# Optimization experiments

Measured on AMD Instinct MI355X. Metric: run time of the kernel, lower is better.

The kernel has to match this reference:

```python
import jax, jax.numpy as jnp
import numpy as np

N_ENT = 50000
N_REL = 16
N_EDGE = 1000000
D = 64


def setup_inputs() -> dict:
    key = jax.random.key(0)
    ks = jax.random.split(key, 20)
    inp = {
        'ent_embed': jax.random.normal(ks[0], (N_ENT, D), jnp.float32) * 0.1,
        'rel_embed': jax.random.normal(ks[1], (N_REL, D), jnp.float32) * 0.1,
        'W_R': jax.random.normal(ks[2], (N_REL, D, D), jnp.float32) * 0.1,
        'W1_0': jax.random.normal(ks[3], (64, 64), jnp.float32) * 0.1,
        'b1_0': jax.random.normal(ks[4], (64,), jnp.float32) * 0.1,
        'W2_0': jax.random.normal(ks[5], (64, 64), jnp.float32) * 0.1,
        'b2_0': jax.random.normal(ks[6], (64,), jnp.float32) * 0.1,
        'W1_1': jax.random.normal(ks[7], (64, 32), jnp.float32) * 0.1,
        'b1_1': jax.random.normal(ks[8], (32,), jnp.float32) * 0.1,
        'W2_1': jax.random.normal(ks[9], (64, 32), jnp.float32) * 0.1,
        'b2_1': jax.random.normal(ks[10], (32,), jnp.float32) * 0.1,
        'W1_2': jax.random.normal(ks[11], (32, 16), jnp.float32) * 0.1,
        'b1_2': jax.random.normal(ks[12], (16,), jnp.float32) * 0.1,
        'W2_2': jax.random.normal(ks[13], (32, 16), jnp.float32) * 0.1,
        'b2_2': jax.random.normal(ks[14], (16,), jnp.float32) * 0.1,
        'src': jax.random.randint(ks[15], (N_EDGE,), 0, N_ENT, jnp.int32),
        'dst': jax.random.randint(ks[16], (N_EDGE,), 0, N_ENT, jnp.int32),
        'etype': jax.random.randint(ks[17], (N_EDGE,), 0, N_REL, jnp.int32),
    }
    return inp


def _l2_normalize(x, eps=1e-12):
    # matches torch F.normalize(p=2, dim=1)
    n = jnp.sqrt(jnp.sum(x * x, axis=1, keepdims=True))
    return x / jnp.maximum(n, eps)


def _kgat_forward(ent_embed, rel_embed, W_R, layer_params, src, dst, etype):
    N = ent_embed.shape[0]
    # --- compute_attention: per-relation TransR projection of all entities ---
    # equivalent to per-edge ent[src] @ W_R[type] without materializing [E, D, D]
    proj = jnp.einsum('nd,rde->rne', ent_embed, W_R)          # [R, N, D]
    r_mul_t = proj[etype, src]                                # [E, D] (tail = src)
    r_mul_h = proj[etype, dst]                                # [E, D] (head = dst)
    att = jnp.sum(r_mul_t * jnp.tanh(r_mul_h + rel_embed[etype]), axis=-1)  # [E]
    # edge softmax grouped by destination node
    m = jax.ops.segment_max(att, dst, num_segments=N)         # [N]
    e = jnp.exp(att - m[dst])
    s = jax.ops.segment_sum(e, dst, num_segments=N)           # [N]
    a = e / s[dst]                                            # [E]

    # --- cf_embedding: bi-interaction aggregator layers ---
    h = ent_embed
    all_embed = [h]
    for (W1, b1, W2, b2) in layer_params:
        msg = a[:, None] * h[src]                             # [E, d_in]
        N_h = jax.ops.segment_sum(msg, dst, num_segments=N)   # [N, d_in]
        out = (jax.nn.leaky_relu((h + N_h) @ W1 + b1, 0.01)
               + jax.nn.leaky_relu((h * N_h) @ W2 + b2, 0.01))
        h = out
        all_embed.append(_l2_normalize(out))
    return jnp.concatenate(all_embed, axis=1)                 # [N, 64+64+32+16=176]


def reference(ent_embed, rel_embed, W_R,
              W1_0, b1_0, W2_0, b2_0,
              W1_1, b1_1, W2_1, b2_1,
              W1_2, b1_2, W2_2, b2_2,
              src, dst, etype):
    layer_params = [(W1_0, b1_0, W2_0, b2_0),
                    (W1_1, b1_1, W2_1, b2_1),
                    (W1_2, b1_2, W2_2, b2_2)]
    return _kgat_forward(ent_embed, rel_embed, W_R, layer_params, src, dst, etype)
```

## Files before the change

kernel.cpp:

```cpp
#include <hip/hip_runtime.h>
#include <hip/hip_bf16.h>
#include <cmath>

#define N_ENT  50000
#define N_RELS 16
#define N_EDGE 1000000
#define DIM    64
#define OUT_STRIDE 176

typedef float f32x4 __attribute__((ext_vector_type(4)));
typedef short s16x8 __attribute__((ext_vector_type(8)));
typedef uint  u32x4 __attribute__((ext_vector_type(4)));

__device__ inline void bf16x8_unpack(uint4 u, float* f) {
    f[0] = __uint_as_float((u.x & 0xffffu) << 16);
    f[1] = __uint_as_float(u.x & 0xffff0000u);
    f[2] = __uint_as_float((u.y & 0xffffu) << 16);
    f[3] = __uint_as_float(u.y & 0xffff0000u);
    f[4] = __uint_as_float((u.z & 0xffffu) << 16);
    f[5] = __uint_as_float(u.z & 0xffff0000u);
    f[6] = __uint_as_float((u.w & 0xffffu) << 16);
    f[7] = __uint_as_float(u.w & 0xffff0000u);
}

__device__ inline ushort f2bf(float x) {
    __hip_bfloat16 b = __float2bfloat16(x);
    return *(ushort*)&b;
}

__device__ inline uint cvt_pk_bf16(float lo, float hi) {
    uint r;
    asm("v_cvt_pk_bf16_f32 %0, %1, %2" : "=v"(r) : "v"(lo), "v"(hi));
    return r;
}

__device__ __host__ inline int pcol(int p) {
    int qp = (p >> 3) & 7;
    int k  = p & 7;
    return 16 * (k >> 1) + 2 * qp + (k & 1);
}

__global__ __launch_bounds__(256) void prep_convert_kernel(
        const float* __restrict__ ent,
        ushort* __restrict__ ent_pi,
        float* __restrict__ out) {
    int i = blockIdx.x * blockDim.x + threadIdx.x;
    if (i < N_ENT * DIM) {
        float v = ent[i];
        ushort b = f2bf(v);
        int n = i >> 6, c = i & 63;
        int pos = ((c & 15) >> 1) * 8 + ((c >> 4) << 1) + (c & 1);
        ent_pi[(size_t)n * 64 + pos] = b;
        out[(size_t)n * OUT_STRIDE + c] = v;
    }
}

__global__ __launch_bounds__(256) void scan1_kernel(
        const int* __restrict__ counts, int* __restrict__ excl,
        int* __restrict__ bsum, int n) {
    __shared__ int sh[256];
    int t = threadIdx.x;
    int i = blockIdx.x * 256 + t;
    int c = (i < n) ? counts[i] : 0;
    sh[t] = c;
    __syncthreads();
    for (int off = 1; off < 256; off <<= 1) {
        int v = (t >= off) ? sh[t - off] : 0;
        __syncthreads();
        sh[t] += v;
        __syncthreads();
    }
    if (i < n) excl[i] = sh[t] - c;
    if (t == 255) bsum[blockIdx.x] = sh[255];
}

__global__ __launch_bounds__(256) void scan2_kernel(
        const int* __restrict__ bsum, int* __restrict__ boff,
        int* __restrict__ row_ptr, int nb, int n) {
    __shared__ int sh[256];
    int t = threadIdx.x;
    int v = (t < nb) ? bsum[t] : 0;
    sh[t] = v;
    __syncthreads();
    for (int off = 1; off < 256; off <<= 1) {
        int x = (t >= off) ? sh[t - off] : 0;
        __syncthreads();
        sh[t] += x;
        __syncthreads();
    }
    if (t < nb) boff[t] = sh[t] - v;
    if (t == nb - 1) row_ptr[n] = sh[t];
}

__global__ __launch_bounds__(256) void scan3_pos_kernel(
        const int* __restrict__ excl, const int* __restrict__ boff,
        int* __restrict__ row_ptr,
        const int* __restrict__ src, const int* __restrict__ dst,
        const int* __restrict__ etype, const int* __restrict__ off,
        unsigned long long* __restrict__ einfo) {
    int i = blockIdx.x * blockDim.x + threadIdx.x;
    if (i < N_ENT) row_ptr[i] = excl[i] + boff[i >> 8];
    if (i < N_EDGE) {
        int d = dst[i];
        int pos = excl[d] + boff[d >> 8] + off[i];
        unsigned long long info =
              (unsigned long long)(unsigned)src[i]
            | ((unsigned long long)(unsigned)d << 16)
            | ((unsigned long long)(unsigned)etype[i] << 32);
        einfo[pos] = info;
    }
}

__device__ __forceinline__ void gz_body(
        int r, int wid, int nw, int lane,
        const ushort* __restrict__ ent_pi,
        const float*  __restrict__ W_R,
        const float*  __restrict__ rel,
        ushort* __restrict__ Z,
        float* __restrict__ myLds) {
    int m = lane & 15;
    int q = lane >> 4;

    const float* Wr = W_R + (size_t)r * DIM * DIM;
    s16x8 b1[4][2], b2[4][2];
#pragma unroll
    for (int c = 0; c < 4; ++c)
#pragma unroll
        for (int ch = 0; ch < 2; ++ch)
#pragma unroll
            for (int j = 0; j < 8; ++j) {
                b1[c][ch][j] = (short)f2bf(Wr[pcol(ch * 32 + q * 8 + j) * DIM + c * 16 + m]);
                b2[c][ch][j] = (short)f2bf(Wr[(c * 16 + m) * DIM + ch * 32 + q * 8 + j]);
            }
    float relv[4];
#pragma unroll
    for (int c = 0; c < 4; ++c) relv[c] = rel[r * DIM + c * 16 + m];

    int par = m & 1;
    const int ntiles = N_ENT / 16;

    for (int t = wid; t < ntiles; t += nw) {
        int row0 = t * 16;
        const s16x8* arow = (const s16x8*)(ent_pi + (size_t)(row0 + m) * DIM);
        s16x8 a0 = arow[q];
        s16x8 a1 = arow[4 + q];
        f32x4 acc[4];
#pragma unroll
        for (int c = 0; c < 4; ++c) acc[c] = (f32x4){0.f, 0.f, 0.f, 0.f};
#pragma unroll
        for (int c = 0; c < 4; ++c) {
            acc[c] = __builtin_amdgcn_mfma_f32_16x16x32_bf16(a0, b1[c][0], acc[c], 0, 0, 0);
            acc[c] = __builtin_amdgcn_mfma_f32_16x16x32_bf16(a1, b1[c][1], acc[c], 0, 0, 0);
        }
#pragma unroll
        for (int c = 0; c < 4; ++c)
#pragma unroll
            for (int i = 0; i < 4; ++i) {
                float x = acc[c][i] + relv[c];
                float e2 = __expf(2.f * x);
                float g = 1.f - 2.f * __builtin_amdgcn_rcpf(e2 + 1.f);
                myLds[(q * 4 + i) * 68 + c * 16 + m] = g;
            }
        union { uint u[4]; s16x8 v; } a2u[2];
#pragma unroll
        for (int ch = 0; ch < 2; ++ch) {
            const f32x4* gp = (const f32x4*)(myLds + m * 68 + ch * 32 + q * 8);
            f32x4 g0 = gp[0];
            f32x4 g1 = gp[1];
            a2u[ch].u[0] = cvt_pk_bf16(g0[0], g0[1]);
            a2u[ch].u[1] = cvt_pk_bf16(g0[2], g0[3]);
            a2u[ch].u[2] = cvt_pk_bf16(g1[0], g1[1]);
            a2u[ch].u[3] = cvt_pk_bf16(g1[2], g1[3]);
        }

        f32x4 zacc[4];
#pragma unroll
        for (int c = 0; c < 4; ++c) zacc[c] = (f32x4){0.f, 0.f, 0.f, 0.f};
#pragma unroll
        for (int c = 0; c < 4; ++c) {
            zacc[c] = __builtin_amdgcn_mfma_f32_16x16x32_bf16(a2u[0].v, b2[c][0], zacc[c], 0, 0, 0);
            zacc[c] = __builtin_amdgcn_mfma_f32_16x16x32_bf16(a2u[1].v, b2[c][1], zacc[c], 0, 0, 0);
        }

        int rowA = row0 + 4 * q + (par ? 2 : 0);
        ushort* zb = Z + ((size_t)r * N_ENT + rowA) * 64 + (m >> 1) * 8;
#pragma unroll
        for (int rep = 0; rep < 2; ++rep) {
            u32x4 Wv;
#pragma unroll
            for (int c = 0; c < 4; ++c) {
                float send = par ? zacc[c][rep] : zacc[c][2 + rep];
                float own  = par ? zacc[c][2 + rep] : zacc[c][rep];
                float oth  = __shfl_xor(send, 1, 64);
                float lo = par ? oth : own;
                float hi = par ? own : oth;
                Wv[c] = cvt_pk_bf16(lo, hi);
            }
            __builtin_nontemporal_store(Wv, (u32x4*)(zb + rep * 64));
        }
    }
}

#define HIST_LANES 131072

__global__ __launch_bounds__(256, 4) void gz_hist_kernel(
        const ushort* __restrict__ ent_pi,
        const float*  __restrict__ W_R,
        const float*  __restrict__ rel,
        ushort* __restrict__ Z,
        const int* __restrict__ dst,
        int* __restrict__ counts,
        int* __restrict__ off) {
    __shared__ __align__(16) float lds[3][16 * 68 + 16];
    int lane = threadIdx.x & 63;
    int wv   = threadIdx.x >> 6;

    if (wv == 3) {
        int lane_gid = blockIdx.x * 64 + lane;
        int d[8]; bool v[8]; int o[8];
#pragma unroll
        for (int k = 0; k < 8; ++k) {
            int i = lane_gid + k * HIST_LANES;
            v[k] = (i < N_EDGE);
            d[k] = v[k] ? dst[i] : 0;
        }
#pragma unroll
        for (int k = 0; k < 8; ++k)
            if (v[k]) o[k] = atomicAdd(&counts[d[k]], 1);
#pragma unroll
        for (int k = 0; k < 8; ++k)
            if (v[k]) off[lane_gid + k * HIST_LANES] = o[k];
        return;
    }

    int r   = blockIdx.x >> 7;
    int xb  = blockIdx.x & 127;
    int wid = xb * 3 + wv;
    gz_body(r, wid, 384, lane, ent_pi, W_R, rel, Z, lds[wv]);
}

__global__ __launch_bounds__(256) void att_dot_kernel(
        const ushort* __restrict__ ent_pi,
        const ushort* __restrict__ Z,
        const unsigned long long* __restrict__ einfo,
        uint2* __restrict__ es_csr,
        int n_edge) {
    int tid  = blockIdx.x * blockDim.x + threadIdx.x;
    int lane = threadIdx.x & 63;
    int sub  = lane >> 3;
    int q    = lane & 7;
    int base = (tid >> 6) * 64;
    if (base >= n_edge) return;

    int e[8];
    unsigned long long inf[8];
#pragma unroll
    for (int k = 0; k < 8; ++k) {
        e[k] = base + k * 8 + sub;
        inf[k] = (e[k] < n_edge) ? einfo[e[k]] : 0ull;
    }

    uint4 uz[8], ue[8];
#pragma unroll
    for (int k = 0; k < 8; ++k) {
        int s = (int)(inf[k] & 0xffffu);
        int d = (int)((inf[k] >> 16) & 0xffffu);
        int r = (int)((inf[k] >> 32) & 0xfu);
        uz[k] = *(const uint4*)(Z + ((size_t)r * N_ENT + d) * DIM + q * 8);
        ue[k] = *(const uint4*)(ent_pi + (size_t)s * DIM + q * 8);
    }

    float pr[8];
#pragma unroll
    for (int k = 0; k < 8; ++k) {
        float zv[8], ev[8];
        bf16x8_unpack(uz[k], zv);
        bf16x8_unpack(ue[k], ev);
        float p = 0.f;
#pragma unroll
        for (int j = 0; j < 8; ++j) p = fmaf(ev[j], zv[j], p);
        pr[k] = p;
    }
#pragma unroll
    for (int k = 0; k < 8; ++k) {
        pr[k] += __shfl_xor(pr[k], 1, 64);
        pr[k] += __shfl_xor(pr[k], 2, 64);
        pr[k] += __shfl_xor(pr[k], 4, 64);
    }

    if (q == 0) {
#pragma unroll
        for (int k = 0; k < 8; ++k)
            if (e[k] < n_edge)
                es_csr[e[k]] = make_uint2(__float_as_uint(pr[k]),
                                          (unsigned)(inf[k] & 0xffffu));
    }
}

__global__ __launch_bounds__(256) void agg64s_kernel(
        const ushort* __restrict__ tab,
        const uint2* __restrict__ es_csr,
        const int* __restrict__ row_ptr,
        float2* __restrict__ stats,
        float* __restrict__ N_h, int n_node) {
    int wid  = (blockIdx.x * blockDim.x + threadIdx.x) >> 6;
    int lane = threadIdx.x & 63;
    if (wid >= n_node) return;
    int q   = lane & 7;
    int sub = lane >> 3;

    int start = row_ptr[wid], end = row_ptr[wid + 1];

    float mx = -INFINITY;
    for (int i = start + lane; i < end; i += 64)
        mx = fmaxf(mx, __uint_as_float(es_csr[i].x));
#pragma unroll
    for (int o = 32; o > 0; o >>= 1)
        mx = fmaxf(mx, __shfl_xor(mx, o, 64));
    float ssum = 0.f;
    for (int i = start + lane; i < end; i += 64)
        ssum += __expf(__uint_as_float(es_csr[i].x) - mx);
#pragma unroll
    for (int o = 32; o > 0; o >>= 1)
        ssum += __shfl_xor(ssum, o, 64);
    float inv = (end > start) ? (1.0f / ssum) : 0.f;
    if (lane == 0) stats[wid] = make_float2(mx, inv);

    float acc[8];
#pragma unroll
    for (int j = 0; j < 8; ++j) acc[j] = 0.f;

    for (int p = start + sub; p < end; p += 8) {
        uint2 es = es_csr[p];
        float av = __expf(__uint_as_float(es.x) - mx);
        int   si = (int)es.y;
        uint4 u  = *(const uint4*)(tab + (size_t)si * 64 + q * 8);
        float g[8];
        bf16x8_unpack(u, g);
#pragma unroll
        for (int j = 0; j < 8; ++j) acc[j] = fmaf(av, g[j], acc[j]);
    }
#pragma unroll
    for (int mask = 8; mask < 64; mask <<= 1)
#pragma unroll
        for (int j = 0; j < 8; ++j)
            acc[j] += __shfl_xor(acc[j], mask, 64);

    if (sub == 0) {
        float* dstp = N_h + (size_t)wid * 64 + q * 8;
        *(float4*)(dstp)     = (float4){acc[0] * inv, acc[1] * inv, acc[2] * inv, acc[3] * inv};
        *(float4*)(dstp + 4) = (float4){acc[4] * inv, acc[5] * inv, acc[6] * inv, acc[7] * inv};
    }
}

__global__ __launch_bounds__(256) void agg64_kernel(
        const ushort* __restrict__ tab,
        const uint2* __restrict__ es_csr,
        const int* __restrict__ row_ptr,
        const float2* __restrict__ stats,
        float* __restrict__ N_h, int n_node) {
    int wid  = (blockIdx.x * blockDim.x + threadIdx.x) >> 6;
    int lane = threadIdx.x & 63;
    if (wid >= n_node) return;
    int q   = lane & 7;
    int sub = lane >> 3;

    int start = row_ptr[wid], end = row_ptr[wid + 1];
    float2 st = stats[wid];
    float mx = st.x, inv = st.y;
    float acc[8];
#pragma unroll
    for (int j = 0; j < 8; ++j) acc[j] = 0.f;

    for (int p = start + sub; p < end; p += 8) {
        uint2 es = es_csr[p];
        float av = __expf(__uint_as_float(es.x) - mx);
        int   si = (int)es.y;
        uint4 u  = *(const uint4*)(tab + (size_t)si * 64 + q * 8);
        float g[8];
        bf16x8_unpack(u, g);
#pragma unroll
        for (int j = 0; j < 8; ++j) acc[j] = fmaf(av, g[j], acc[j]);
    }
#pragma unroll
    for (int mask = 8; mask < 64; mask <<= 1)
#pragma unroll
        for (int j = 0; j < 8; ++j)
            acc[j] += __shfl_xor(acc[j], mask, 64);

    if (sub == 0) {
        float* dstp = N_h + (size_t)wid * 64 + q * 8;
        *(float4*)(dstp)     = (float4){acc[0] * inv, acc[1] * inv, acc[2] * inv, acc[3] * inv};
        *(float4*)(dstp + 4) = (float4){acc[4] * inv, acc[5] * inv, acc[6] * inv, acc[7] * inv};
    }
}

__global__ __launch_bounds__(256) void agg32_kernel(
        const ushort* __restrict__ tab,
        const uint2* __restrict__ es_csr,
        const int* __restrict__ row_ptr,
        const float2* __restrict__ stats,
        float* __restrict__ N_h, int n_node) {
    int wid  = (blockIdx.x * blockDim.x + threadIdx.x) >> 6;
    int lane = threadIdx.x & 63;
    if (wid >= n_node) return;
    int q   = lane & 3;
    int sub = lane >> 2;

    int start = row_ptr[wid], end = row_ptr[wid + 1];
    float2 st = stats[wid];
    float mx = st.x, inv = st.y;
    float acc[8];
#pragma unroll
    for (int j = 0; j < 8; ++j) acc[j] = 0.f;

    for (int p = start + sub; p < end; p += 16) {
        uint2 es = es_csr[p];
        float av = __expf(__uint_as_float(es.x) - mx);
        int   si = (int)es.y;
        uint4 u  = *(const uint4*)(tab + (size_t)si * 32 + q * 8);
        float g[8];
        bf16x8_unpack(u, g);
#pragma unroll
        for (int j = 0; j < 8; ++j) acc[j] = fmaf(av, g[j], acc[j]);
    }
#pragma unroll
    for (int mask = 4; mask < 64; mask <<= 1)
#pragma unroll
        for (int j = 0; j < 8; ++j)
            acc[j] += __shfl_xor(acc[j], mask, 64);

    if (sub == 0) {
        float* dstp = N_h + (size_t)wid * 32 + q * 8;
        *(float4*)(dstp)     = (float4){acc[0] * inv, acc[1] * inv, acc[2] * inv, acc[3] * inv};
        *(float4*)(dstp + 4) = (float4){acc[4] * inv, acc[5] * inv, acc[6] * inv, acc[7] * inv};
    }
}

template <int D_IN, int D_OUT, bool PERM>
__global__ __launch_bounds__(256) void mlp_mfma_kernel(
        const ushort* __restrict__ h,
        const float* __restrict__ N_h,
        const float* __restrict__ W1, const float* __restrict__ b1,
        const float* __restrict__ W2, const float* __restrict__ b2,
        ushort* __restrict__ ho,
        float* __restrict__ out_buf, int out_col) {
    constexpr int CH = D_IN / 32;
    constexpr int CT = D_OUT / 16;

    int lane = threadIdx.x & 63;
    int m    = lane & 15;
    int q    = lane >> 4;
    int wid  = blockIdx.x * (blockDim.x >> 6) + (threadIdx.x >> 6);
    int nw   = gridDim.x * (blockDim.x >> 6);

    s16x8 bu[CT][CH], bv[CT][CH];
#pragma unroll
    for (int c = 0; c < CT; ++c)
#pragma unroll
        for (int ch = 0; ch < CH; ++ch)
#pragma unroll
            for (int j = 0; j < 8; ++j) {
                int p = ch * 32 + q * 8 + j;
                int k = PERM ? pcol(p) : p;
                bu[c][ch][j] = (short)f2bf(W1[k * D_OUT + c * 16 + m]);
                bv[c][ch][j] = (short)f2bf(W2[k * D_OUT + c * 16 + m]);
            }

    const int ntiles = N_ENT / 16;
    for (int t = wid; t < ntiles; t += nw) {
        int row0 = t * 16;
        s16x8 au[CH], av[CH];
#pragma unroll
        for (int ch = 0; ch < CH; ++ch) {
            uint4 hu = *(const uint4*)(h + (size_t)(row0 + m) * D_IN + ch * 32 + q * 8);
            float hv8[8];
            bf16x8_unpack(hu, hv8);
            const float4* np = (const float4*)(N_h + (size_t)(row0 + m) * D_IN + ch * 32 + q * 8);
            float4 na = np[0], nb = np[1];
            float nv[8] = {na.x, na.y, na.z, na.w, nb.x, nb.y, nb.z, nb.w};
#pragma unroll
            for (int j = 0; j < 8; ++j) {
                au[ch][j] = (short)f2bf(hv8[j] + nv[j]);
                av[ch][j] = (short)f2bf(hv8[j] * nv[j]);
            }
        }

        f32x4 accu[CT], accv[CT];
#pragma unroll
        for (int c = 0; c < CT; ++c) {
            accu[c] = (f32x4){0.f, 0.f, 0.f, 0.f};
            accv[c] = (f32x4){0.f, 0.f, 0.f, 0.f};
        }
#pragma unroll
        for (int c = 0; c < CT; ++c)
#pragma unroll
            for (int ch = 0; ch < CH; ++ch) {
                accu[c] = __builtin_amdgcn_mfma_f32_16x16x32_bf16(au[ch], bu[c][ch], accu[c], 0, 0, 0);
                accv[c] = __builtin_amdgcn_mfma_f32_16x16x32_bf16(av[ch], bv[c][ch], accv[c], 0, 0, 0);
            }

        float res[CT][4];
        float sq[4] = {0.f, 0.f, 0.f, 0.f};
#pragma unroll
        for (int c = 0; c < CT; ++c) {
            float bb1 = b1[c * 16 + m];
            float bb2 = b2[c * 16 + m];
#pragma unroll
            for (int i = 0; i < 4; ++i) {
                float o1 = accu[c][i] + bb1;
                float o2 = accv[c][i] + bb2;
                float r1 = (o1 >= 0.f) ? o1 : 0.01f * o1;
                float r2 = (o2 >= 0.f) ? o2 : 0.01f * o2;
                float rr = r1 + r2;
                res[c][i] = rr;
                sq[i] = fmaf(rr, rr, sq[i]);
            }
        }
#pragma unroll
        for (int mask = 1; mask < 16; mask <<= 1)
#pragma unroll
            for (int i = 0; i < 4; ++i)
                sq[i] += __shfl_xor(sq[i], mask, 64);

#pragma unroll
        for (int i = 0; i < 4; ++i) {
            int row = row0 + q * 4 + i;
            float inv = 1.f / fmaxf(sqrtf(sq[i]), 1e-12f);
#pragma unroll
            for (int c = 0; c < CT; ++c) {
                int col = c * 16 + m;
                out_buf[(size_t)row * OUT_STRIDE + out_col + col] = res[c][i] * inv;
                if (ho) ho[(size_t)row * D_OUT + col] = f2bf(res[c][i]);
            }
        }
    }
}

extern "C" void kernel_launch(void* const* d_in, const int* in_sizes, int n_in,
                              void* d_out, int out_size, void* d_ws, size_t ws_size,
                              hipStream_t stream) {
    const float* ent  = (const float*)d_in[0];
    const float* rel  = (const float*)d_in[1];
    const float* W_R  = (const float*)d_in[2];
    const float* W1_0 = (const float*)d_in[3];
    const float* b1_0 = (const float*)d_in[4];
    const float* W2_0 = (const float*)d_in[5];
    const float* b2_0 = (const float*)d_in[6];
    const float* W1_1 = (const float*)d_in[7];
    const float* b1_1 = (const float*)d_in[8];
    const float* W2_1 = (const float*)d_in[9];
    const float* b2_1 = (const float*)d_in[10];
    const float* W1_2 = (const float*)d_in[11];
    const float* b1_2 = (const float*)d_in[12];
    const float* W2_2 = (const float*)d_in[13];
    const float* b2_2 = (const float*)d_in[14];
    const int*   src   = (const int*)d_in[15];
    const int*   dst   = (const int*)d_in[16];
    const int*   etype = (const int*)d_in[17];
    float* out = (float*)d_out;

    char* w = (char*)d_ws;
    uint2*  es_csr  = (uint2*)w;  w += (size_t)N_EDGE * 8;
    int*    counts  = (int*)w;    w += (size_t)(N_ENT + 64) * 4;
    int*    row_ptr = (int*)w;    w += (size_t)(N_ENT + 64) * 4;
    float2* stats   = (float2*)w; w += (size_t)(N_ENT + 64) * 8;
    int*    excl    = (int*)w;    w += (size_t)(N_ENT + 64) * 4;
    int*    bsum    = (int*)w;    w += 256 * 4;
    int*    boff    = (int*)w;    w += 256 * 4;
    ushort* ent_pi  = (ushort*)w; w += (size_t)N_ENT * 64 * 2;
    ushort* h1      = (ushort*)w; w += (size_t)N_ENT * 64 * 2;
    ushort* h2      = (ushort*)w; w += (size_t)N_ENT * 32 * 2;
    float*  N_h     = (float*)w;  w += (size_t)N_ENT * 64 * 4;
    ushort* Z       = (ushort*)w;
    (void)ws_size;

    int* off = (int*)es_csr;
    unsigned long long* einfo = (unsigned long long*)N_h;

    hipMemsetAsync(counts, 0, (size_t)N_ENT * 4, stream);

    const int nb = (N_ENT + 255) / 256;

    prep_convert_kernel<<<(N_ENT * DIM + 255) / 256, 256, 0, stream>>>(
        ent, ent_pi, out);

    gz_hist_kernel<<<2048, 256, 0, stream>>>(
        ent_pi, W_R, rel, Z, dst, counts, off);

    scan1_kernel<<<nb, 256, 0, stream>>>(counts, excl, bsum, N_ENT);
    scan2_kernel<<<1, 256, 0, stream>>>(bsum, boff, row_ptr, nb, N_ENT);
    scan3_pos_kernel<<<(N_EDGE + 255) / 256, 256, 0, stream>>>(
        excl, boff, row_ptr, src, dst, etype, off, einfo);

    att_dot_kernel<<<((N_EDGE + 63) / 64 * 64 + 255) / 256, 256, 0, stream>>>(
        ent_pi, Z, einfo, es_csr, N_EDGE);

    const int aggGrid = (N_ENT + 3) / 4;
    const int mlpGrid = 782;

    agg64s_kernel<<<aggGrid, 256, 0, stream>>>(ent_pi, es_csr, row_ptr, stats, N_h, N_ENT);
    mlp_mfma_kernel<64, 64, true><<<mlpGrid, 256, 0, stream>>>(
        ent_pi, N_h, W1_0, b1_0, W2_0, b2_0, h1, out, 64);

    agg64_kernel<<<aggGrid, 256, 0, stream>>>(h1, es_csr, row_ptr, stats, N_h, N_ENT);
    mlp_mfma_kernel<64, 32, false><<<mlpGrid, 256, 0, stream>>>(
        h1, N_h, W1_1, b1_1, W2_1, b2_1, h2, out, 128);

    agg32_kernel<<<aggGrid, 256, 0, stream>>>(h2, es_csr, row_ptr, stats, N_h, N_ENT);
    mlp_mfma_kernel<32, 16, false><<<mlpGrid, 256, 0, stream>>>(
        h2, N_h, W1_2, b1_2, W2_2, b2_2, nullptr, out, 160);
}
```

Baseline: 358.5 us.

## Fuse neighbor aggregation with bi-interaction MLP per node

Merges each layer's aggregation kernel and MFMA MLP kernel into one persistent kernel. Each wavefront aggregates one node's neighbours, stages h and N_h in shared memory, and computes the small MLP with scalar FMAs against bf16 weights held in LDS. This removes the fp32 N_h round trip through global memory and three kernel launches. In exchange it drops MFMA for scalar dot products and adds weight staging into LDS in every block. The LDS handoff relies only on an lgkmcnt wait, with no barrier, for intra-wave visibility. einfo gets its own workspace buffer now that N_h is gone.

```diff
diff --git a/kernel.cpp b/kernel.cpp
--- a/kernel.cpp
+++ b/kernel.cpp
@@ -297,242 +297,132 @@
     }
 }
 
-__global__ __launch_bounds__(256) void agg64s_kernel(
+template <int D_IN, int D_OUT, bool STATS, bool PERM>
+__global__ __launch_bounds__(256) void agg_mlp_kernel(
         const ushort* __restrict__ tab,
         const uint2* __restrict__ es_csr,
         const int* __restrict__ row_ptr,
         float2* __restrict__ stats,
-        float* __restrict__ N_h, int n_node) {
-    int wid  = (blockIdx.x * blockDim.x + threadIdx.x) >> 6;
-    int lane = threadIdx.x & 63;
-    if (wid >= n_node) return;
-    int q   = lane & 7;
-    int sub = lane >> 3;
-
-    int start = row_ptr[wid], end = row_ptr[wid + 1];
-
-    float mx = -INFINITY;
-    for (int i = start + lane; i < end; i += 64)
-        mx = fmaxf(mx, __uint_as_float(es_csr[i].x));
-#pragma unroll
-    for (int o = 32; o > 0; o >>= 1)
-        mx = fmaxf(mx, __shfl_xor(mx, o, 64));
-    float ssum = 0.f;
-    for (int i = start + lane; i < end; i += 64)
-        ssum += __expf(__uint_as_float(es_csr[i].x) - mx);
-#pragma unroll
-    for (int o = 32; o > 0; o >>= 1)
-        ssum += __shfl_xor(ssum, o, 64);
-    float inv = (end > start) ? (1.0f / ssum) : 0.f;
-    if (lane == 0) stats[wid] = make_float2(mx, inv);
-
-    float acc[8];
-#pragma unroll
-    for (int j = 0; j < 8; ++j) acc[j] = 0.f;
-
-    for (int p = start + sub; p < end; p += 8) {
-        uint2 es = es_csr[p];
-        float av = __expf(__uint_as_float(es.x) - mx);
-        int   si = (int)es.y;
-        uint4 u  = *(const uint4*)(tab + (size_t)si * 64 + q * 8);
-        float g[8];
-        bf16x8_unpack(u, g);
-#pragma unroll
-        for (int j = 0; j < 8; ++j) acc[j] = fmaf(av, g[j], acc[j]);
-    }
-#pragma unroll
-    for (int mask = 8; mask < 64; mask <<= 1)
-#pragma unroll
-        for (int j = 0; j < 8; ++j)
-            acc[j] += __shfl_xor(acc[j], mask, 64);
-
-    if (sub == 0) {
-        float* dstp = N_h + (size_t)wid * 64 + q * 8;
-        *(float4*)(dstp)     = (float4){acc[0] * inv, acc[1] * inv, acc[2] * inv, acc[3] * inv};
-        *(float4*)(dstp + 4) = (float4){acc[4] * inv, acc[5] * inv, acc[6] * inv, acc[7] * inv};
-    }
-}
-
-__global__ __launch_bounds__(256) void agg64_kernel(
-        const ushort* __restrict__ tab,
-        const uint2* __restrict__ es_csr,
-        const int* __restrict__ row_ptr,
-        const float2* __restrict__ stats,
-        float* __restrict__ N_h, int n_node) {
-    int wid  = (blockIdx.x * blockDim.x + threadIdx.x) >> 6;
-    int lane = threadIdx.x & 63;
-    if (wid >= n_node) return;
-    int q   = lane & 7;
-    int sub = lane >> 3;
-
-    int start = row_ptr[wid], end = row_ptr[wid + 1];
-    float2 st = stats[wid];
-    float mx = st.x, inv = st.y;
-    float acc[8];
-#pragma unroll
-    for (int j = 0; j < 8; ++j) acc[j] = 0.f;
-
-    for (int p = start + sub; p < end; p += 8) {
-        uint2 es = es_csr[p];
-        float av = __expf(__uint_as_float(es.x) - mx);
-        int   si = (int)es.y;
-        uint4 u  = *(const uint4*)(tab + (size_t)si * 64 + q * 8);
-        float g[8];
-        bf16x8_unpack(u, g);
-#pragma unroll
-        for (int j = 0; j < 8; ++j) acc[j] = fmaf(av, g[j], acc[j]);
-    }
-#pragma unroll
-    for (int mask = 8; mask < 64; mask <<= 1)
-#pragma unroll
-        for (int j = 0; j < 8; ++j)
-            acc[j] += __shfl_xor(acc[j], mask, 64);
-
-    if (sub == 0) {
-        float* dstp = N_h + (size_t)wid * 64 + q * 8;
-        *(float4*)(dstp)     = (float4){acc[0] * inv, acc[1] * inv, acc[2] * inv, acc[3] * inv};
-        *(float4*)(dstp + 4) = (float4){acc[4] * inv, acc[5] * inv, acc[6] * inv, acc[7] * inv};
-    }
-}
-
-__global__ __launch_bounds__(256) void agg32_kernel(
-        const ushort* __restrict__ tab,
-        const uint2* __restrict__ es_csr,
-        const int* __restrict__ row_ptr,
-        const float2* __restrict__ stats,
-        float* __restrict__ N_h, int n_node) {
-    int wid  = (blockIdx.x * blockDim.x + threadIdx.x) >> 6;
-    int lane = threadIdx.x & 63;
-    if (wid >= n_node) return;
-    int q   = lane & 3;
-    int sub = lane >> 2;
-
-    int start = row_ptr[wid], end = row_ptr[wid + 1];
-    float2 st = stats[wid];
-    float mx = st.x, inv = st.y;
-    float acc[8];
-#pragma unroll
-    for (int j = 0; j < 8; ++j) acc[j] = 0.f;
-
-    for (int p = start + sub; p < end; p += 16) {
-        uint2 es = es_csr[p];
-        float av = __expf(__uint_as_float(es.x) - mx);
-        int   si = (int)es.y;
-        uint4 u  = *(const uint4*)(tab + (size_t)si * 32 + q * 8);
-        float g[8];
-        bf16x8_unpack(u, g);
-#pragma unroll
-        for (int j = 0; j < 8; ++j) acc[j] = fmaf(av, g[j], acc[j]);
-    }
-#pragma unroll
-    for (int mask = 4; mask < 64; mask <<= 1)
-#pragma unroll
-        for (int j = 0; j < 8; ++j)
-            acc[j] += __shfl_xor(acc[j], mask, 64);
-
-    if (sub == 0) {
-        float* dstp = N_h + (size_t)wid * 32 + q * 8;
-        *(float4*)(dstp)     = (float4){acc[0] * inv, acc[1] * inv, acc[2] * inv, acc[3] * inv};
-        *(float4*)(dstp + 4) = (float4){acc[4] * inv, acc[5] * inv, acc[6] * inv, acc[7] * inv};
-    }
-}
-
-template <int D_IN, int D_OUT, bool PERM>
-__global__ __launch_bounds__(256) void mlp_mfma_kernel(
-        const ushort* __restrict__ h,
-        const float* __restrict__ N_h,
         const float* __restrict__ W1, const float* __restrict__ b1,
         const float* __restrict__ W2, const float* __restrict__ b2,
         ushort* __restrict__ ho,
-        float* __restrict__ out_buf, int out_col) {
-    constexpr int CH = D_IN / 32;
-    constexpr int CT = D_OUT / 16;
-
-    int lane = threadIdx.x & 63;
-    int m    = lane & 15;
-    int q    = lane >> 4;
-    int wid  = blockIdx.x * (blockDim.x >> 6) + (threadIdx.x >> 6);
-    int nw   = gridDim.x * (blockDim.x >> 6);
-
-    s16x8 bu[CT][CH], bv[CT][CH];
-#pragma unroll
-    for (int c = 0; c < CT; ++c)
-#pragma unroll
-        for (int ch = 0; ch < CH; ++ch)
-#pragma unroll
-            for (int j = 0; j < 8; ++j) {
-                int p = ch * 32 + q * 8 + j;
-                int k = PERM ? pcol(p) : p;
-                bu[c][ch][j] = (short)f2bf(W1[k * D_OUT + c * 16 + m]);
-                bv[c][ch][j] = (short)f2bf(W2[k * D_OUT + c * 16 + m]);
-            }
-
-    const int ntiles = N_ENT / 16;
-    for (int t = wid; t < ntiles; t += nw) {
-        int row0 = t * 16;
-        s16x8 au[CH], av[CH];
-#pragma unroll
-        for (int ch = 0; ch < CH; ++ch) {
-            uint4 hu = *(const uint4*)(h + (size_t)(row0 + m) * D_IN + ch * 32 + q * 8);
-            float hv8[8];
-            bf16x8_unpack(hu, hv8);
-            const float4* np = (const float4*)(N_h + (size_t)(row0 + m) * D_IN + ch * 32 + q * 8);
-            float4 na = np[0], nb = np[1];
-            float nv[8] = {na.x, na.y, na.z, na.w, nb.x, nb.y, nb.z, nb.w};
-#pragma unroll
-            for (int j = 0; j < 8; ++j) {
-                au[ch][j] = (short)f2bf(hv8[j] + nv[j]);
-                av[ch][j] = (short)f2bf(hv8[j] * nv[j]);
-            }
-        }
-
-        f32x4 accu[CT], accv[CT];
-#pragma unroll
-        for (int c = 0; c < CT; ++c) {
-            accu[c] = (f32x4){0.f, 0.f, 0.f, 0.f};
-            accv[c] = (f32x4){0.f, 0.f, 0.f, 0.f};
-        }
-#pragma unroll
-        for (int c = 0; c < CT; ++c)
-#pragma unroll
-            for (int ch = 0; ch < CH; ++ch) {
-                accu[c] = __builtin_amdgcn_mfma_f32_16x16x32_bf16(au[ch], bu[c][ch], accu[c], 0, 0, 0);
-                accv[c] = __builtin_amdgcn_mfma_f32_16x16x32_bf16(av[ch], bv[c][ch], accv[c], 0, 0, 0);
-            }
-
-        float res[CT][4];
-        float sq[4] = {0.f, 0.f, 0.f, 0.f};
-#pragma unroll
-        for (int c = 0; c < CT; ++c) {
-            float bb1 = b1[c * 16 + m];
-            float bb2 = b2[c * 16 + m];
-#pragma unroll
-            for (int i = 0; i < 4; ++i) {
-                float o1 = accu[c][i] + bb1;
-                float o2 = accv[c][i] + bb2;
-                float r1 = (o1 >= 0.f) ? o1 : 0.01f * o1;
-                float r2 = (o2 >= 0.f) ? o2 : 0.01f * o2;
-                float rr = r1 + r2;
-                res[c][i] = rr;
-                sq[i] = fmaf(rr, rr, sq[i]);
-            }
-        }
-#pragma unroll
-        for (int mask = 1; mask < 16; mask <<= 1)
-#pragma unroll
-            for (int i = 0; i < 4; ++i)
-                sq[i] += __shfl_xor(sq[i], mask, 64);
-
-#pragma unroll
-        for (int i = 0; i < 4; ++i) {
-            int row = row0 + q * 4 + i;
-            float inv = 1.f / fmaxf(sqrtf(sq[i]), 1e-12f);
-#pragma unroll
-            for (int c = 0; c < CT; ++c) {
-                int col = c * 16 + m;
-                out_buf[(size_t)row * OUT_STRIDE + out_col + col] = res[c][i] * inv;
-                if (ho) ho[(size_t)row * D_OUT + col] = f2bf(res[c][i]);
-            }
+        float* __restrict__ out_buf, int out_col, int n_node) {
+    constexpr int LPR = D_IN / 8;
+    constexpr int EPW = 64 / LPR;
+    constexpr int GRP = 64 / D_OUT;
+    constexpr int KP  = D_IN / GRP;
+
+    __shared__ __align__(16) ushort w1s[D_IN * D_OUT];
+    __shared__ __align__(16) ushort w2s[D_IN * D_OUT];
+    __shared__ __align__(16) float rows[4][2][64];
+
+    int t = threadIdx.x;
+    for (int i = t; i < D_IN * D_OUT; i += 256) {
+        int k = i / D_OUT, j = i % D_OUT;
+        int kk = PERM ? pcol(k) : k;
+        int slot = (k >> 1) * (2 * D_OUT) + 2 * j + (k & 1);
+        w1s[slot] = f2bf(W1[kk * D_OUT + j]);
+        w2s[slot] = f2bf(W2[kk * D_OUT + j]);
+    }
+    __syncthreads();
+
+    int wv   = t >> 6;
+    int lane = t & 63;
+    int q    = lane % LPR;
+    int sub  = lane / LPR;
+    int j    = lane % D_OUT;
+    int g    = lane / D_OUT;
+    float bb1 = b1[j], bb2 = b2[j];
+    float* hr = rows[wv][0];
+    float* nr = rows[wv][1];
+
+    for (int wid = blockIdx.x * 4 + wv; wid < n_node; wid += gridDim.x * 4) {
+        int start = row_ptr[wid], end = row_ptr[wid + 1];
+
+        float mx, inv;
+        if (STATS) {
+            mx = -INFINITY;
+            for (int i = start + lane; i < end; i += 64)
+                mx = fmaxf(mx, __uint_as_float(es_csr[i].x));
+#pragma unroll
+            for (int o = 32; o > 0; o >>= 1)
+                mx = fmaxf(mx, __shfl_xor(mx, o, 64));
+            float ssum = 0.f;
+            for (int i = start + lane; i < end; i += 64)
+                ssum += __expf(__uint_as_float(es_csr[i].x) - mx);
+#pragma unroll
+            for (int o = 32; o > 0; o >>= 1)
+                ssum += __shfl_xor(ssum, o, 64);
+            inv = (end > start) ? (1.0f / ssum) : 0.f;
+            if (lane == 0) stats[wid] = make_float2(mx, inv);
+        } else {
+            float2 st = stats[wid];
+            mx = st.x; inv = st.y;
+        }
+
+        float acc[8];
+#pragma unroll
+        for (int k = 0; k < 8; ++k) acc[k] = 0.f;
+        for (int p = start + sub; p < end; p += EPW) {
+            uint2 es = es_csr[p];
+            float av = __expf(__uint_as_float(es.x) - mx);
+            int   si = (int)es.y;
+            uint4 u  = *(const uint4*)(tab + (size_t)si * D_IN + q * 8);
+            float gg[8];
+            bf16x8_unpack(u, gg);
+#pragma unroll
+            for (int k = 0; k < 8; ++k) acc[k] = fmaf(av, gg[k], acc[k]);
+        }
+#pragma unroll
+        for (int mask = LPR; mask < 64; mask <<= 1)
+#pragma unroll
+            for (int k = 0; k < 8; ++k)
+                acc[k] += __shfl_xor(acc[k], mask, 64);
+
+        if (lane < LPR) {
+#pragma unroll
+            for (int k = 0; k < 8; ++k) nr[lane * 8 + k] = acc[k] * inv;
+            uint4 hu = *(const uint4*)(tab + (size_t)wid * D_IN + lane * 8);
+            float hv[8];
+            bf16x8_unpack(hu, hv);
+#pragma unroll
+            for (int k = 0; k < 8; ++k) hr[lane * 8 + k] = hv[k];
+        }
+        asm volatile("s_waitcnt lgkmcnt(0)" ::: "memory");
+
+        float o1 = 0.f, o2 = 0.f;
+#pragma unroll
+        for (int k = g * KP; k < g * KP + KP; k += 2) {
+            float2 hv = *(float2*)&hr[k];
+            float2 nv = *(float2*)&nr[k];
+            uint w1p = *(uint*)&w1s[(k >> 1) * (2 * D_OUT) + 2 * j];
+            uint w2p = *(uint*)&w2s[(k >> 1) * (2 * D_OUT) + 2 * j];
+            float w1a = __uint_as_float((w1p & 0xffffu) << 16);
+            float w1b = __uint_as_float(w1p & 0xffff0000u);
+            float w2a = __uint_as_float((w2p & 0xffffu) << 16);
+            float w2b = __uint_as_float(w2p & 0xffff0000u);
+            o1 = fmaf(hv.x + nv.x, w1a, o1);
+            o1 = fmaf(hv.y + nv.y, w1b, o1);
+            o2 = fmaf(hv.x * nv.x, w2a, o2);
+            o2 = fmaf(hv.y * nv.y, w2b, o2);
+        }
+#pragma unroll
+        for (int mask = D_OUT; mask < 64; mask <<= 1) {
+            o1 += __shfl_xor(o1, mask, 64);
+            o2 += __shfl_xor(o2, mask, 64);
+        }
+        o1 += bb1; o2 += bb2;
+        float r1 = (o1 >= 0.f) ? o1 : 0.01f * o1;
+        float r2 = (o2 >= 0.f) ? o2 : 0.01f * o2;
+        float rr = r1 + r2;
+        float part = (g == 0) ? rr * rr : 0.f;
+#pragma unroll
+        for (int mask = 1; mask < 64; mask <<= 1)
+            part += __shfl_xor(part, mask, 64);
+        float invn = 1.f / fmaxf(sqrtf(part), 1e-12f);
+        if (g == 0) {
+            out_buf[(size_t)wid * OUT_STRIDE + out_col + j] = rr * invn;
+            if (ho) ho[(size_t)wid * D_OUT + j] = f2bf(rr);
         }
     }
 }
@@ -562,6 +452,8 @@
 
     char* w = (char*)d_ws;
     uint2*  es_csr  = (uint2*)w;  w += (size_t)N_EDGE * 8;
+    unsigned long long* einfo = (unsigned long long*)w;
+    w += (size_t)N_EDGE * 8;
     int*    counts  = (int*)w;    w += (size_t)(N_ENT + 64) * 4;
     int*    row_ptr = (int*)w;    w += (size_t)(N_ENT + 64) * 4;
     float2* stats   = (float2*)w; w += (size_t)(N_ENT + 64) * 8;
@@ -571,12 +463,10 @@
     ushort* ent_pi  = (ushort*)w; w += (size_t)N_ENT * 64 * 2;
     ushort* h1      = (ushort*)w; w += (size_t)N_ENT * 64 * 2;
     ushort* h2      = (ushort*)w; w += (size_t)N_ENT * 32 * 2;
-    float*  N_h     = (float*)w;  w += (size_t)N_ENT * 64 * 4;
     ushort* Z       = (ushort*)w;
     (void)ws_size;
 
     int* off = (int*)es_csr;
-    unsigned long long* einfo = (unsigned long long*)N_h;
 
     hipMemsetAsync(counts, 0, (size_t)N_ENT * 4, stream);
 
@@ -596,18 +486,10 @@
     att_dot_kernel<<<((N_EDGE + 63) / 64 * 64 + 255) / 256, 256, 0, stream>>>(
         ent_pi, Z, einfo, es_csr, N_EDGE);
 
-    const int aggGrid = (N_ENT + 3) / 4;
-    const int mlpGrid = 782;
-
-    agg64s_kernel<<<aggGrid, 256, 0, stream>>>(ent_pi, es_csr, row_ptr, stats, N_h, N_ENT);
-    mlp_mfma_kernel<64, 64, true><<<mlpGrid, 256, 0, stream>>>(
-        ent_pi, N_h, W1_0, b1_0, W2_0, b2_0, h1, out, 64);
-
-    agg64_kernel<<<aggGrid, 256, 0, stream>>>(h1, es_csr, row_ptr, stats, N_h, N_ENT);
-    mlp_mfma_kernel<64, 32, false><<<mlpGrid, 256, 0, stream>>>(
-        h1, N_h, W1_1, b1_1, W2_1, b2_1, h2, out, 128);
-
-    agg32_kernel<<<aggGrid, 256, 0, stream>>>(h2, es_csr, row_ptr, stats, N_h, N_ENT);
-    mlp_mfma_kernel<32, 16, false><<<mlpGrid, 256, 0, stream>>>(
-        h2, N_h, W1_2, b1_2, W2_2, b2_2, nullptr, out, 160);
-}
+    agg_mlp_kernel<64, 64, true,  true ><<<4096, 256, 0, stream>>>(
+        ent_pi, es_csr, row_ptr, stats, W1_0, b1_0, W2_0, b2_0, h1, out, 64, N_ENT);
+    agg_mlp_kernel<64, 32, false, false><<<4096, 256, 0, stream>>>(
+        h1, es_csr, row_ptr, stats, W1_1, b1_1, W2_1, b2_1, h2, out, 128, N_ENT);
+    agg_mlp_kernel<32, 16, false, false><<<4096, 256, 0, stream>>>(
+        h2, es_csr, row_ptr, stats, W1_2, b1_2, W2_2, b2_2, nullptr, out, 160, N_ENT);
+}
```

Result: slower. 416.9 us (+16.3%).

## Compute TransR tanh per edge from projected table and cache normalized attention

Applied to the files above, without the earlier changes.

Replaces the per-relation second projection (tanh then multiply by W_R transpose) with storing only the projected entity table P, and evaluates tanh(P[dst]+rel)·P[src] per edge in the attention kernel. This removes one MFMA GEMM and the LDS staging from the gz kernel. It moves the transcendental work to the 1M edges, which is slightly more exps. Separately, the first aggregation writes the normalized softmax weight back into the CSR, so later layers skip the exp and the stats buffer.

```diff
diff --git a/kernel.cpp b/kernel.cpp
--- a/kernel.cpp
+++ b/kernel.cpp
@@ -42,7 +42,9 @@
 
 __global__ __launch_bounds__(256) void prep_convert_kernel(
         const float* __restrict__ ent,
+        const float* __restrict__ rel,
         ushort* __restrict__ ent_pi,
+        ushort* __restrict__ rel_pi,
         float* __restrict__ out) {
     int i = blockIdx.x * blockDim.x + threadIdx.x;
     if (i < N_ENT * DIM) {
@@ -52,6 +54,11 @@
         int pos = ((c & 15) >> 1) * 8 + ((c >> 4) << 1) + (c & 1);
         ent_pi[(size_t)n * 64 + pos] = b;
         out[(size_t)n * OUT_STRIDE + c] = v;
+    }
+    if (i < N_RELS * DIM) {
+        int r = i >> 6, c = i & 63;
+        int pos = ((c & 15) >> 1) * 8 + ((c >> 4) << 1) + (c & 1);
+        rel_pi[r * 64 + pos] = f2bf(rel[i]);
     }
 }
 
@@ -111,30 +118,23 @@
     }
 }
 
-__device__ __forceinline__ void gz_body(
+__device__ __forceinline__ void p_body(
         int r, int wid, int nw, int lane,
         const ushort* __restrict__ ent_pi,
         const float*  __restrict__ W_R,
-        const float*  __restrict__ rel,
-        ushort* __restrict__ Z,
-        float* __restrict__ myLds) {
+        ushort* __restrict__ P) {
     int m = lane & 15;
     int q = lane >> 4;
 
     const float* Wr = W_R + (size_t)r * DIM * DIM;
-    s16x8 b1[4][2], b2[4][2];
+    s16x8 b1[4][2];
 #pragma unroll
     for (int c = 0; c < 4; ++c)
 #pragma unroll
         for (int ch = 0; ch < 2; ++ch)
 #pragma unroll
-            for (int j = 0; j < 8; ++j) {
+            for (int j = 0; j < 8; ++j)
                 b1[c][ch][j] = (short)f2bf(Wr[pcol(ch * 32 + q * 8 + j) * DIM + c * 16 + m]);
-                b2[c][ch][j] = (short)f2bf(Wr[(c * 16 + m) * DIM + ch * 32 + q * 8 + j]);
-            }
-    float relv[4];
-#pragma unroll
-    for (int c = 0; c < 4; ++c) relv[c] = rel[r * DIM + c * 16 + m];
 
     int par = m & 1;
     const int ntiles = N_ENT / 16;
@@ -152,51 +152,22 @@
             acc[c] = __builtin_amdgcn_mfma_f32_16x16x32_bf16(a0, b1[c][0], acc[c], 0, 0, 0);
             acc[c] = __builtin_amdgcn_mfma_f32_16x16x32_bf16(a1, b1[c][1], acc[c], 0, 0, 0);
         }
-#pragma unroll
-        for (int c = 0; c < 4; ++c)
-#pragma unroll
-            for (int i = 0; i < 4; ++i) {
-                float x = acc[c][i] + relv[c];
-                float e2 = __expf(2.f * x);
-                float g = 1.f - 2.f * __builtin_amdgcn_rcpf(e2 + 1.f);
-                myLds[(q * 4 + i) * 68 + c * 16 + m] = g;
-            }
-        union { uint u[4]; s16x8 v; } a2u[2];
-#pragma unroll
-        for (int ch = 0; ch < 2; ++ch) {
-            const f32x4* gp = (const f32x4*)(myLds + m * 68 + ch * 32 + q * 8);
-            f32x4 g0 = gp[0];
-            f32x4 g1 = gp[1];
-            a2u[ch].u[0] = cvt_pk_bf16(g0[0], g0[1]);
-            a2u[ch].u[1] = cvt_pk_bf16(g0[2], g0[3]);
-            a2u[ch].u[2] = cvt_pk_bf16(g1[0], g1[1]);
-            a2u[ch].u[3] = cvt_pk_bf16(g1[2], g1[3]);
-        }
-
-        f32x4 zacc[4];
-#pragma unroll
-        for (int c = 0; c < 4; ++c) zacc[c] = (f32x4){0.f, 0.f, 0.f, 0.f};
-#pragma unroll
-        for (int c = 0; c < 4; ++c) {
-            zacc[c] = __builtin_amdgcn_mfma_f32_16x16x32_bf16(a2u[0].v, b2[c][0], zacc[c], 0, 0, 0);
-            zacc[c] = __builtin_amdgcn_mfma_f32_16x16x32_bf16(a2u[1].v, b2[c][1], zacc[c], 0, 0, 0);
-        }
 
         int rowA = row0 + 4 * q + (par ? 2 : 0);
-        ushort* zb = Z + ((size_t)r * N_ENT + rowA) * 64 + (m >> 1) * 8;
+        ushort* pb = P + ((size_t)r * N_ENT + rowA) * 64 + (m >> 1) * 8;
 #pragma unroll
         for (int rep = 0; rep < 2; ++rep) {
             u32x4 Wv;
 #pragma unroll
             for (int c = 0; c < 4; ++c) {
-                float send = par ? zacc[c][rep] : zacc[c][2 + rep];
-                float own  = par ? zacc[c][2 + rep] : zacc[c][rep];
+                float send = par ? acc[c][rep] : acc[c][2 + rep];
+                float own  = par ? acc[c][2 + rep] : acc[c][rep];
                 float oth  = __shfl_xor(send, 1, 64);
                 float lo = par ? oth : own;
                 float hi = par ? own : oth;
                 Wv[c] = cvt_pk_bf16(lo, hi);
             }
-            __builtin_nontemporal_store(Wv, (u32x4*)(zb + rep * 64));
+            __builtin_nontemporal_store(Wv, (u32x4*)(pb + rep * 64));
         }
     }
 }
@@ -206,12 +177,10 @@
 __global__ __launch_bounds__(256, 4) void gz_hist_kernel(
         const ushort* __restrict__ ent_pi,
         const float*  __restrict__ W_R,
-        const float*  __restrict__ rel,
-        ushort* __restrict__ Z,
+        ushort* __restrict__ P,
         const int* __restrict__ dst,
         int* __restrict__ counts,
         int* __restrict__ off) {
-    __shared__ __align__(16) float lds[3][16 * 68 + 16];
     int lane = threadIdx.x & 63;
     int wv   = threadIdx.x >> 6;
 
@@ -236,12 +205,12 @@
     int r   = blockIdx.x >> 7;
     int xb  = blockIdx.x & 127;
     int wid = xb * 3 + wv;
-    gz_body(r, wid, 384, lane, ent_pi, W_R, rel, Z, lds[wv]);
+    p_body(r, wid, 384, lane, ent_pi, W_R, P);
 }
 
 __global__ __launch_bounds__(256) void att_dot_kernel(
-        const ushort* __restrict__ ent_pi,
-        const ushort* __restrict__ Z,
+        const ushort* __restrict__ P,
+        const ushort* __restrict__ rel_pi,
         const unsigned long long* __restrict__ einfo,
         uint2* __restrict__ es_csr,
         int n_edge) {
@@ -266,19 +235,26 @@
         int s = (int)(inf[k] & 0xffffu);
         int d = (int)((inf[k] >> 16) & 0xffffu);
         int r = (int)((inf[k] >> 32) & 0xfu);
-        uz[k] = *(const uint4*)(Z + ((size_t)r * N_ENT + d) * DIM + q * 8);
-        ue[k] = *(const uint4*)(ent_pi + (size_t)s * DIM + q * 8);
+        uz[k] = *(const uint4*)(P + ((size_t)r * N_ENT + d) * DIM + q * 8);
+        ue[k] = *(const uint4*)(P + ((size_t)r * N_ENT + s) * DIM + q * 8);
     }
 
     float pr[8];
 #pragma unroll
     for (int k = 0; k < 8; ++k) {
-        float zv[8], ev[8];
+        int r = (int)((inf[k] >> 32) & 0xfu);
+        uint4 ur = *(const uint4*)(rel_pi + r * 64 + q * 8);
+        float zv[8], ev[8], rl[8];
         bf16x8_unpack(uz[k], zv);
         bf16x8_unpack(ue[k], ev);
+        bf16x8_unpack(ur, rl);
         float p = 0.f;
 #pragma unroll
-        for (int j = 0; j < 8; ++j) p = fmaf(ev[j], zv[j], p);
+        for (int j = 0; j < 8; ++j) {
+            float x = zv[j] + rl[j];
+            float g = 1.f - 2.f * __builtin_amdgcn_rcpf(__expf(2.f * x) + 1.f);
+            p = fmaf(ev[j], g, p);
+        }
         pr[k] = p;
     }
 #pragma unroll
@@ -299,9 +275,8 @@
 
 __global__ __launch_bounds__(256) void agg64s_kernel(
         const ushort* __restrict__ tab,
-        const uint2* __restrict__ es_csr,
+        uint2* __restrict__ es_csr,
         const int* __restrict__ row_ptr,
-        float2* __restrict__ stats,
         float* __restrict__ N_h, int n_node) {
     int wid  = (blockIdx.x * blockDim.x + threadIdx.x) >> 6;
     int lane = threadIdx.x & 63;
@@ -324,7 +299,6 @@
     for (int o = 32; o > 0; o >>= 1)
         ssum += __shfl_xor(ssum, o, 64);
     float inv = (end > start) ? (1.0f / ssum) : 0.f;
-    if (lane == 0) stats[wid] = make_float2(mx, inv);
 
     float acc[8];
 #pragma unroll
@@ -332,8 +306,9 @@
 
     for (int p = start + sub; p < end; p += 8) {
         uint2 es = es_csr[p];
-        float av = __expf(__uint_as_float(es.x) - mx);
+        float av = __expf(__uint_as_float(es.x) - mx) * inv;
         int   si = (int)es.y;
+        if (q == 0) es_csr[p].x = __float_as_uint(av);
         uint4 u  = *(const uint4*)(tab + (size_t)si * 64 + q * 8);
         float g[8];
         bf16x8_unpack(u, g);
@@ -348,8 +323,8 @@
 
     if (sub == 0) {
         float* dstp = N_h + (size_t)wid * 64 + q * 8;
-        *(float4*)(dstp)     = (float4){acc[0] * inv, acc[1] * inv, acc[2] * inv, acc[3] * inv};
-        *(float4*)(dstp + 4) = (float4){acc[4] * inv, acc[5] * inv, acc[6] * inv, acc[7] * inv};
+        *(float4*)(dstp)     = (float4){acc[0], acc[1], acc[2], acc[3]};
+        *(float4*)(dstp + 4) = (float4){acc[4], acc[5], acc[6], acc[7]};
     }
 }
 
@@ -357,7 +332,6 @@
         const ushort* __restrict__ tab,
         const uint2* __restrict__ es_csr,
         const int* __restrict__ row_ptr,
-        const float2* __restrict__ stats,
         float* __restrict__ N_h, int n_node) {
     int wid  = (blockIdx.x * blockDim.x + threadIdx.x) >> 6;
     int lane = threadIdx.x & 63;
@@ -366,15 +340,13 @@
     int sub = lane >> 3;
 
     int start = row_ptr[wid], end = row_ptr[wid + 1];
-    float2 st = stats[wid];
-    float mx = st.x, inv = st.y;
     float acc[8];
 #pragma unroll
     for (int j = 0; j < 8; ++j) acc[j] = 0.f;
 
     for (int p = start + sub; p < end; p += 8) {
         uint2 es = es_csr[p];
-        float av = __expf(__uint_as_float(es.x) - mx);
+        float av = __uint_as_float(es.x);
         int   si = (int)es.y;
         uint4 u  = *(const uint4*)(tab + (size_t)si * 64 + q * 8);
         float g[8];
@@ -390,8 +362,8 @@
 
     if (sub == 0) {
         float* dstp = N_h + (size_t)wid * 64 + q * 8;
-        *(float4*)(dstp)     = (float4){acc[0] * inv, acc[1] * inv, acc[2] * inv, acc[3] * inv};
-        *(float4*)(dstp + 4) = (float4){acc[4] * inv, acc[5] * inv, acc[6] * inv, acc[7] * inv};
+        *(float4*)(dstp)     = (float4){acc[0], acc[1], acc[2], acc[3]};
+        *(float4*)(dstp + 4) = (float4){acc[4], acc[5], acc[6], acc[7]};
     }
 }
 
@@ -399,7 +371,6 @@
         const ushort* __restrict__ tab,
         const uint2* __restrict__ es_csr,
         const int* __restrict__ row_ptr,
-        const float2* __restrict__ stats,
         float* __restrict__ N_h, int n_node) {
     int wid  = (blockIdx.x * blockDim.x + threadIdx.x) >> 6;
     int lane = threadIdx.x & 63;
@@ -408,15 +379,13 @@
     int sub = lane >> 2;
 
     int start = row_ptr[wid], end = row_ptr[wid + 1];
-    float2 st = stats[wid];
-    float mx = st.x, inv = st.y;
     float acc[8];
 #pragma unroll
     for (int j = 0; j < 8; ++j) acc[j] = 0.f;
 
     for (int p = start + sub; p < end; p += 16) {
         uint2 es = es_csr[p];
-        float av = __expf(__uint_as_float(es.x) - mx);
+        float av = __uint_as_float(es.x);
         int   si = (int)es.y;
         uint4 u  = *(const uint4*)(tab + (size_t)si * 32 + q * 8);
         float g[8];
@@ -432,8 +401,8 @@
 
     if (sub == 0) {
         float* dstp = N_h + (size_t)wid * 32 + q * 8;
-        *(float4*)(dstp)     = (float4){acc[0] * inv, acc[1] * inv, acc[2] * inv, acc[3] * inv};
-        *(float4*)(dstp + 4) = (float4){acc[4] * inv, acc[5] * inv, acc[6] * inv, acc[7] * inv};
+        *(float4*)(dstp)     = (float4){acc[0], acc[1], acc[2], acc[3]};
+        *(float4*)(dstp + 4) = (float4){acc[4], acc[5], acc[6], acc[7]};
     }
 }
 
@@ -564,29 +533,29 @@
     uint2*  es_csr  = (uint2*)w;  w += (size_t)N_EDGE * 8;
     int*    counts  = (int*)w;    w += (size_t)(N_ENT + 64) * 4;
     int*    row_ptr = (int*)w;    w += (size_t)(N_ENT + 64) * 4;
-    float2* stats   = (float2*)w; w += (size_t)(N_ENT + 64) * 8;
     int*    excl    = (int*)w;    w += (size_t)(N_ENT + 64) * 4;
     int*    bsum    = (int*)w;    w += 256 * 4;
     int*    boff    = (int*)w;    w += 256 * 4;
+    ushort* rel_pi  = (ushort*)w; w += (size_t)N_RELS * 64 * 2;
     ushort* ent_pi  = (ushort*)w; w += (size_t)N_ENT * 64 * 2;
     ushort* h1      = (ushort*)w; w += (size_t)N_ENT * 64 * 2;
     ushort* h2      = (ushort*)w; w += (size_t)N_ENT * 32 * 2;
     float*  N_h     = (float*)w;  w += (size_t)N_ENT * 64 * 4;
-    ushort* Z       = (ushort*)w;
+    ushort* P       = (ushort*)w;
     (void)ws_size;
 
     int* off = (int*)es_csr;
     unsigned long long* einfo = (unsigned long long*)N_h;
 
-    hipMemsetAsync(counts, 0, (size_t)N_ENT * 4, stream);
+    (void)hipMemsetAsync(counts, 0, (size_t)N_ENT * 4, stream);
 
     const int nb = (N_ENT + 255) / 256;
 
     prep_convert_kernel<<<(N_ENT * DIM + 255) / 256, 256, 0, stream>>>(
-        ent, ent_pi, out);
+        ent, rel, ent_pi, rel_pi, out);
 
     gz_hist_kernel<<<2048, 256, 0, stream>>>(
-        ent_pi, W_R, rel, Z, dst, counts, off);
+        ent_pi, W_R, P, dst, counts, off);
 
     scan1_kernel<<<nb, 256, 0, stream>>>(counts, excl, bsum, N_ENT);
     scan2_kernel<<<1, 256, 0, stream>>>(bsum, boff, row_ptr, nb, N_ENT);
@@ -594,20 +563,20 @@
         excl, boff, row_ptr, src, dst, etype, off, einfo);
 
     att_dot_kernel<<<((N_EDGE + 63) / 64 * 64 + 255) / 256, 256, 0, stream>>>(
-        ent_pi, Z, einfo, es_csr, N_EDGE);
+        P, rel_pi, einfo, es_csr, N_EDGE);
 
     const int aggGrid = (N_ENT + 3) / 4;
     const int mlpGrid = 782;
 
-    agg64s_kernel<<<aggGrid, 256, 0, stream>>>(ent_pi, es_csr, row_ptr, stats, N_h, N_ENT);
+    agg64s_kernel<<<aggGrid, 256, 0, stream>>>(ent_pi, es_csr, row_ptr, N_h, N_ENT);
     mlp_mfma_kernel<64, 64, true><<<mlpGrid, 256, 0, stream>>>(
         ent_pi, N_h, W1_0, b1_0, W2_0, b2_0, h1, out, 64);
 
-    agg64_kernel<<<aggGrid, 256, 0, stream>>>(h1, es_csr, row_ptr, stats, N_h, N_ENT);
+    agg64_kernel<<<aggGrid, 256, 0, stream>>>(h1, es_csr, row_ptr, N_h, N_ENT);
     mlp_mfma_kernel<64, 32, false><<<mlpGrid, 256, 0, stream>>>(
         h1, N_h, W1_1, b1_1, W2_1, b2_1, h2, out, 128);
 
-    agg32_kernel<<<aggGrid, 256, 0, stream>>>(h2, es_csr, row_ptr, stats, N_h, N_ENT);
+    agg32_kernel<<<aggGrid, 256, 0, stream>>>(h2, es_csr, row_ptr, N_h, N_ENT);
     mlp_mfma_kernel<32, 16, false><<<mlpGrid, 256, 0, stream>>>(
         h2, N_h, W1_2, b1_2, W2_2, b2_2, nullptr, out, 160);
 }
```

Result: no change. 364.3 us (+1.6%).
